# Kernel optimization log

Measured on AMD Instinct MI355X. Metric: run time of the kernel, lower is better.

The kernel has to match this reference:

```python
import jax, jax.numpy as jnp
import numpy as np

B, S, D_EMB, D_HEAD = 4, 4096, 1024, 64

def setup_inputs() -> dict:
    key = jax.random.key(0)
    kx, kq, kk, kv = jax.random.split(key, 4)
    x = jax.random.normal(kx, (B, S, D_EMB), dtype=jnp.float32)
    # Linear(d_emb -> d_head, bias=False); stored as [d_emb, d_head] so y = x @ W
    sc = 1.0 / np.sqrt(D_EMB)
    Wq = jax.random.normal(kq, (D_EMB, D_HEAD), dtype=jnp.float32) * sc
    Wk = jax.random.normal(kk, (D_EMB, D_HEAD), dtype=jnp.float32) * sc
    Wv = jax.random.normal(kv, (D_EMB, D_HEAD), dtype=jnp.float32) * sc
    return {"x": x, "Wq": Wq, "Wk": Wk, "Wv": Wv}

def reference(x, Wq, Wk, Wv):
    # x: [B, S, D_EMB]
    n = x.shape[1]
    d_head = Wq.shape[1]
    q = x @ Wq  # [B, S, d_head]
    k = x @ Wk
    v = x @ Wv
    w = jnp.einsum('bqd,bkd->bqk', q, k)  # raw scores [B, S, S]
    causal = jnp.tril(jnp.ones((n, n), dtype=bool))
    w = jnp.where(causal[None, :, :], w, -jnp.inf)
    # NOTE: original scales AFTER masking (-inf * scale stays -inf, so math matches SDPA)
    scale = jnp.asarray(d_head, w.dtype) ** -0.5
    w = jax.nn.softmax(w * scale, axis=-1)
    # dropout_p = 0.0 (eval-mode reference)
    return w @ v  # [B, S, d_head]
```

## Files before the change

kernel.cpp:

```cpp
#include <hip/hip_runtime.h>

typedef __attribute__((ext_vector_type(4))) float f32x4;
typedef __attribute__((ext_vector_type(8))) short bf16x8;

#define S_LEN 4096

__device__ inline short f2bf(float f) {
    union { float f; unsigned u; } v; v.f = f;
    unsigned r = (v.u + 0x7fffu + ((v.u >> 16) & 1u)) >> 16;
    return (short)r;
}
__device__ inline unsigned pack2bf(float a, float b) {
    return (unsigned)(unsigned short)f2bf(a) | ((unsigned)(unsigned short)f2bf(b) << 16);
}
__device__ inline unsigned cvt_pk_bf16(float lo, float hi) {
    unsigned r;
    asm("v_cvt_pk_bf16_f32 %0, %1, %2" : "=v"(r) : "v"(lo), "v"(hi));
    return r;
}
__device__ inline void gload_lds16(const void* g, void* l) {
    __builtin_amdgcn_global_load_lds(
        (const __attribute__((address_space(1))) unsigned int*)g,
        (__attribute__((address_space(3))) unsigned int*)l, 16, 0, 0);
}

__global__ __launch_bounds__(256) void wconv_kernel(const float* __restrict__ Wq,
        const float* __restrict__ Wk, const float* __restrict__ Wv,
        short* __restrict__ Wsz) {
    int idx = blockIdx.x * 256 + threadIdx.x;
    int t = idx / 6144;
    int rem = idx - t * 6144;
    int g = rem >> 5, kk = rem & 31;
    int k = t * 32 + kk;
    int m = g >> 6, c = g & 63;
    const float* W = (m == 0) ? Wq : (m == 1) ? Wk : Wv;
    Wsz[idx] = f2bf(W[k * 64 + c]);
}

__global__ __launch_bounds__(256, 4) void qkv_kernel(const float* __restrict__ x,
        const short* __restrict__ Wsz, short* __restrict__ Qb,
        short* __restrict__ Ksz, short* __restrict__ Vsz) {
    __shared__ __align__(16) char Bl[2][12288];
    const int tid = threadIdx.x;
    const int wv = tid >> 6, lane = tid & 63;
    const int wr = wv & 1, wc = wv >> 1;
    const int lr = lane & 15, lg = lane >> 4;
    const int rowbase = blockIdx.x * 32 + wr * 16;

    f32x4 acc[6];
#pragma unroll
    for (int i = 0; i < 6; i++) acc[i] = {0.f, 0.f, 0.f, 0.f};

    const float* xrow = x + (size_t)(rowbase + lr) * 1024 + lg * 8;
    const char* wsrc = (const char*)Wsz + tid * 16;

#define STAGEB(t_, buf_)                                                    \
    {                                                                       \
        const char* s_ = wsrc + (t_) * 12288;                               \
        char* d_ = &Bl[(buf_)][tid * 16];                                   \
        gload_lds16(s_,        d_);                                         \
        gload_lds16(s_ + 4096, d_ + 4096);                                  \
        gload_lds16(s_ + 8192, d_ + 8192);                                  \
    }

    STAGEB(0, 0);
    __syncthreads();

#pragma unroll 4
    for (int t = 0; t < 32; t++) {
        if (t + 1 < 32) STAGEB(t + 1, (t + 1) & 1);

        f32x4 a0 = *(const f32x4*)(xrow + t * 32);
        f32x4 a1 = *(const f32x4*)(xrow + t * 32 + 4);
        union { unsigned u[4]; bf16x8 v; } au;
        au.u[0] = cvt_pk_bf16(a0[0], a0[1]);
        au.u[1] = cvt_pk_bf16(a0[2], a0[3]);
        au.u[2] = cvt_pk_bf16(a1[0], a1[1]);
        au.u[3] = cvt_pk_bf16(a1[2], a1[3]);

        const char* Bb = &Bl[t & 1][0];
#pragma unroll
        for (int cf = 0; cf < 6; cf++) {
            int brow = wc * 96 + cf * 16 + lr;
            bf16x8 b = *(const bf16x8*)(Bb + brow * 64 + lg * 16);
            acc[cf] = __builtin_amdgcn_mfma_f32_16x16x32_bf16(au.v, b, acc[cf], 0, 0, 0);
        }
        __syncthreads();
    }
#undef STAGEB

#pragma unroll
    for (int cf = 0; cf < 6; cf++) {
        int gcol = wc * 96 + cf * 16 + lr;
        int m = gcol >> 6, cm = gcol & 63;
#pragma unroll
        for (int r = 0; r < 4; r++) {
            int row = rowbase + lg * 4 + r;
            short bv = f2bf(acc[cf][r]);
            if (m == 0) {
                Qb[(size_t)row * 64 + cm] = bv;
            } else if (m == 1) {
                int b = row >> 12, s12 = row & 4095;
                int tk = s12 >> 6, rr = s12 & 63;
                Ksz[(((size_t)(b * 64 + tk) * 64 + rr) << 6)
                    + (((cm >> 3) ^ (rr & 7)) << 3) + (cm & 7)] = bv;
            } else {
                int b = row >> 12, s12 = row & 4095;
                int tk = s12 >> 6, kk = s12 & 63;
                Vsz[(((size_t)(b * 64 + tk) * 64 + cm) << 6)
                    + (((kk >> 3) ^ (cm & 7)) << 3) + (kk & 7)] = bv;
            }
        }
    }
}

__global__ __launch_bounds__(256, 3) void attn_fused_kernel(const short* __restrict__ Qb,
        const short* __restrict__ Ksz, const short* __restrict__ Vsz,
        float* __restrict__ o_part, float* __restrict__ m_part, float* __restrict__ l_part) {
    __shared__ __align__(16) char kvb2[2][16384];
    __shared__ __align__(16) char Pl[4 * 4096];
    const int tid = threadIdx.x;
    const int wv = tid >> 6, lane = tid & 63;
    const int lr = lane & 15, lg = lane >> 4;

    const int j = blockIdx.x;
    const int bb = j / 272;
    int jb = j - bb * 272;
    int qt = 0;
    while (jb >= ((qt + 2) >> 1)) { jb -= (qt + 2) >> 1; qt++; }
    const int c = jb;
    const int t0 = c * 4;
    const int nb = min(4, 2 * qt + 2 - 4 * c);
    const int qb_w = qt * 128 + wv * 32;

    bf16x8 qa[2][2];
#pragma unroll
    for (int qf = 0; qf < 2; qf++)
#pragma unroll
        for (int dk = 0; dk < 2; dk++)
            qa[qf][dk] = *(const bf16x8*)(Qb + (size_t)(bb * S_LEN + qb_w + qf * 16 + lr) * 64 + dk * 32 + lg * 8);

    f32x4 o[2][4];
    float mrun[2] = {-1e30f, -1e30f}, lrun[2] = {0.f, 0.f};
#pragma unroll
    for (int qf = 0; qf < 2; qf++)
#pragma unroll
        for (int df = 0; df < 4; df++) o[qf][df] = {0.f, 0.f, 0.f, 0.f};

    const char* Kg = (const char*)Ksz;
    const char* Vg = (const char*)Vsz;
    char* Pb = Pl + wv * 4096;

#define STAGEKV(t_, s_)                                                       \
    {                                                                         \
        size_t off_ = (size_t)(bb * 64 + t0 + (t_)) * 8192 + tid * 16;        \
        char* d_ = kvb2[(s_)] + tid * 16;                                     \
        gload_lds16(Kg + off_,        d_);                                    \
        gload_lds16(Kg + off_ + 4096, d_ + 4096);                             \
        gload_lds16(Vg + off_,        d_ + 8192);                             \
        gload_lds16(Vg + off_ + 4096, d_ + 12288);                            \
    }

    STAGEKV(0, 0);
    asm volatile("s_waitcnt vmcnt(0)" ::: "memory");
    __builtin_amdgcn_s_barrier();

    for (int t = 0; t < nb; t++) {
        if (t + 1 < nb) STAGEKV(t + 1, (t + 1) & 1);

        const int kv0 = (t0 + t) * 64;
        if (kv0 <= qb_w + 31) {
            const char* Kl = kvb2[t & 1];
            const char* Vl = Kl + 8192;

            bf16x8 kb[4][2], vb[2][4];
#pragma unroll
            for (int kf = 0; kf < 4; kf++)
#pragma unroll
                for (int dk = 0; dk < 2; dk++) {
                    int r = kf * 16 + lr;
                    kb[kf][dk] = *(const bf16x8*)(Kl + r * 128 + ((((dk << 2) | lg) ^ (r & 7)) << 4));
                }
#pragma unroll
            for (int kk = 0; kk < 2; kk++)
#pragma unroll
                for (int df = 0; df < 4; df++) {
                    int d = df * 16 + lr;
                    vb[kk][df] = *(const bf16x8*)(Vl + d * 128 + ((((kk << 2) | lg) ^ (d & 7)) << 4));
                }

            f32x4 s[2][4];
#pragma unroll
            for (int qf = 0; qf < 2; qf++)
#pragma unroll
                for (int kf = 0; kf < 4; kf++) {
                    f32x4 z = {0.f, 0.f, 0.f, 0.f};
                    z = __builtin_amdgcn_mfma_f32_16x16x32_bf16(kb[kf][0], qa[qf][0], z, 0, 0, 0);
                    s[qf][kf] = __builtin_amdgcn_mfma_f32_16x16x32_bf16(kb[kf][1], qa[qf][1], z, 0, 0, 0);
                }

            const bool needmask = (kv0 + 63) > qb_w;
#pragma unroll
            for (int qf = 0; qf < 2; qf++)
#pragma unroll
                for (int kf = 0; kf < 4; kf++)
#pragma unroll
                    for (int r = 0; r < 4; r++) {
                        float v = s[qf][kf][r] * 0.125f;
                        if (needmask) {
                            int row = qb_w + qf * 16 + lr;
                            int col = kv0 + kf * 16 + lg * 4 + r;
                            if (col > row) v = -1e30f;
                        }
                        s[qf][kf][r] = v;
                    }

#pragma unroll
            for (int qf = 0; qf < 2; qf++) {
                float pm = -1e30f;
#pragma unroll
                for (int kf = 0; kf < 4; kf++)
#pragma unroll
                    for (int r = 0; r < 4; r++) pm = fmaxf(pm, s[qf][kf][r]);
                pm = fmaxf(pm, __shfl_xor(pm, 16, 64));
                pm = fmaxf(pm, __shfl_xor(pm, 32, 64));
                float mnew = fmaxf(mrun[qf], pm);
                float fac = __expf(mrun[qf] - mnew);
                mrun[qf] = mnew;

                const int q = qf * 16 + lr;
                const int swz = (q & 7) << 4;
                float rs = 0.f;
#pragma unroll
                for (int kf = 0; kf < 4; kf++) {
                    float p0 = __expf(s[qf][kf][0] - mnew);
                    float p1 = __expf(s[qf][kf][1] - mnew);
                    float p2 = __expf(s[qf][kf][2] - mnew);
                    float p3 = __expf(s[qf][kf][3] - mnew);
                    rs += (p0 + p1) + (p2 + p3);
                    uint2 w; w.x = pack2bf(p0, p1); w.y = pack2bf(p2, p3);
                    int byt = (q * 128 + kf * 32 + lg * 8) ^ swz;
                    *(uint2*)(Pb + byt) = w;
                }
                rs += __shfl_xor(rs, 16, 64);
                rs += __shfl_xor(rs, 32, 64);
                lrun[qf] = lrun[qf] * fac + rs;
#pragma unroll
                for (int df = 0; df < 4; df++)
#pragma unroll
                    for (int r = 0; r < 4; r++) o[qf][df][r] *= fac;
            }

            bf16x8 pa[2][2];
#pragma unroll
            for (int qf = 0; qf < 2; qf++)
#pragma unroll
                for (int kk = 0; kk < 2; kk++) {
                    int q = qf * 16 + lr;
                    int byt = (q * 128 + kk * 64 + lg * 16) ^ ((q & 7) << 4);
                    pa[qf][kk] = *(const bf16x8*)(Pb + byt);
                }

#pragma unroll
            for (int qf = 0; qf < 2; qf++)
#pragma unroll
                for (int df = 0; df < 4; df++) {
                    o[qf][df] = __builtin_amdgcn_mfma_f32_16x16x32_bf16(vb[0][df], pa[qf][0], o[qf][df], 0, 0, 0);
                    o[qf][df] = __builtin_amdgcn_mfma_f32_16x16x32_bf16(vb[1][df], pa[qf][1], o[qf][df], 0, 0, 0);
                }
        }

        asm volatile("s_waitcnt vmcnt(0)" ::: "memory");
        __builtin_amdgcn_sched_barrier(0);
        __builtin_amdgcn_s_barrier();
    }
#undef STAGEKV

#pragma unroll
    for (int qf = 0; qf < 2; qf++)
#pragma unroll
        for (int df = 0; df < 4; df++)
            *(f32x4*)(o_part + ((size_t)j * 128 + wv * 32 + qf * 16 + lr) * 64 + df * 16 + lg * 4) = o[qf][df];
    if (lg == 0) {
#pragma unroll
        for (int qf = 0; qf < 2; qf++) {
            m_part[(size_t)j * 128 + wv * 32 + qf * 16 + lr] = mrun[qf];
            l_part[(size_t)j * 128 + wv * 32 + qf * 16 + lr] = lrun[qf];
        }
    }
}

__global__ __launch_bounds__(256) void combine_kernel(const float* __restrict__ o_part,
        const float* __restrict__ m_part, const float* __restrict__ l_part,
        float* __restrict__ out) {
    const int idx = blockIdx.x * 256 + threadIdx.x;
    const int col = idx & 63;
    const int rowg = idx >> 6;
    const int bb = rowg >> 12;
    const int srow = rowg & 4095;
    const int qt = srow >> 7;
    const int rloc = srow & 127;
    const int h = qt >> 1;
    const int n = (qt + 2) >> 1;
    const int jb0 = bb * 272 + h * (h + 1) + (qt & 1) * (h + 1);

    float M = -1e30f;
    for (int cc = 0; cc < n; cc++) M = fmaxf(M, m_part[(size_t)(jb0 + cc) * 128 + rloc]);
    float L = 0.f, acc = 0.f;
    for (int cc = 0; cc < n; cc++) {
        float w = __expf(m_part[(size_t)(jb0 + cc) * 128 + rloc] - M);
        L += l_part[(size_t)(jb0 + cc) * 128 + rloc] * w;
        acc += o_part[((size_t)(jb0 + cc) * 128 + rloc) * 64 + col] * w;
    }
    out[idx] = acc / L;
}

extern "C" void kernel_launch(void* const* d_in, const int* in_sizes, int n_in,
                              void* d_out, int out_size, void* d_ws, size_t ws_size,
                              hipStream_t stream) {
    const float* x  = (const float*)d_in[0];
    const float* Wq = (const float*)d_in[1];
    const float* Wk = (const float*)d_in[2];
    const float* Wv = (const float*)d_in[3];
    float* out = (float*)d_out;

    char* ws = (char*)d_ws;
    short* Wsz = (short*)(ws);
    short* Qb  = (short*)(ws + 0x60000);
    short* Ksz = (short*)(ws + 0x260000);
    short* Vsz = (short*)(ws + 0x460000);

    const int njobs = 1088;
    float* o_part = (float*)(ws + 0x660000);
    float* m_part = o_part + (size_t)njobs * 128 * 64;
    float* l_part = m_part + (size_t)njobs * 128;

    hipLaunchKernelGGL(wconv_kernel, dim3(768), dim3(256), 0, stream, Wq, Wk, Wv, Wsz);
    hipLaunchKernelGGL(qkv_kernel,  dim3(512), dim3(256), 0, stream, x, Wsz, Qb, Ksz, Vsz);
    hipLaunchKernelGGL(attn_fused_kernel, dim3(njobs), dim3(256), 0, stream,
                       Qb, Ksz, Vsz, o_part, m_part, l_part);
    hipLaunchKernelGGL(combine_kernel, dim3(4096), dim3(256), 0, stream,
                       o_part, m_part, l_part, out);
}
```

Baseline: 82.61 us.

## Stage x tiles through LDS with triple-buffered async loads in QKV projection

The QKV projection kernel now stages the fp32 x tile into LDS with global_load_lds, using an XOR swizzle, alongside the weight tile. It uses a three-deep buffer ring with a prefetch distance of two, and replaces __syncthreads with explicit vmcnt waits plus a single barrier per iteration. The aim is to hide global load latency for the activation reads, which were previously direct per-lane global loads on the critical path. In exchange, LDS use grows to 48KB per block and the occupancy hint drops from 4 to 2 blocks.

```diff
diff --git a/kernel.cpp b/kernel.cpp
--- a/kernel.cpp
+++ b/kernel.cpp
@@ -37,57 +37,69 @@
     Wsz[idx] = f2bf(W[k * 64 + c]);
 }
 
-__global__ __launch_bounds__(256, 4) void qkv_kernel(const float* __restrict__ x,
+__global__ __launch_bounds__(256, 2) void qkv_kernel(const float* __restrict__ x,
         const short* __restrict__ Wsz, short* __restrict__ Qb,
         short* __restrict__ Ksz, short* __restrict__ Vsz) {
-    __shared__ __align__(16) char Bl[2][12288];
+    __shared__ __align__(16) char lds[3][16384];
     const int tid = threadIdx.x;
     const int wv = tid >> 6, lane = tid & 63;
     const int wr = wv & 1, wc = wv >> 1;
     const int lr = lane & 15, lg = lane >> 4;
-    const int rowbase = blockIdx.x * 32 + wr * 16;
+    const int rowbase = blockIdx.x * 32;
 
     f32x4 acc[6];
 #pragma unroll
     for (int i = 0; i < 6; i++) acc[i] = {0.f, 0.f, 0.f, 0.f};
 
-    const float* xrow = x + (size_t)(rowbase + lr) * 1024 + lg * 8;
+    const int arow = tid >> 3, acL = tid & 7;
+    const char* asrc = (const char*)(x + (size_t)(rowbase + arow) * 1024
+                                     + ((acL ^ (arow & 7)) << 2));
     const char* wsrc = (const char*)Wsz + tid * 16;
 
-#define STAGEB(t_, buf_)                                                    \
+#define STAGE(t_, s_)                                                       \
     {                                                                       \
-        const char* s_ = wsrc + (t_) * 12288;                               \
-        char* d_ = &Bl[(buf_)][tid * 16];                                   \
-        gload_lds16(s_,        d_);                                         \
-        gload_lds16(s_ + 4096, d_ + 4096);                                  \
-        gload_lds16(s_ + 8192, d_ + 8192);                                  \
-    }
-
-    STAGEB(0, 0);
-    __syncthreads();
-
-#pragma unroll 4
+        char* base_ = lds[(s_)];                                            \
+        gload_lds16(asrc + (t_) * 128, base_ + tid * 16);                   \
+        const char* bs_ = wsrc + (t_) * 12288;                              \
+        gload_lds16(bs_,        base_ + 4096 + tid * 16);                   \
+        gload_lds16(bs_ + 4096, base_ + 8192 + tid * 16);                   \
+        gload_lds16(bs_ + 8192, base_ + 12288 + tid * 16);                  \
+    }
+
+    STAGE(0, 0);
+    STAGE(1, 1);
+
+    const int rowA = wr * 16 + lr;
+    const int aswz = rowA & 7;
+
+#pragma unroll
     for (int t = 0; t < 32; t++) {
-        if (t + 1 < 32) STAGEB(t + 1, (t + 1) & 1);
-
-        f32x4 a0 = *(const f32x4*)(xrow + t * 32);
-        f32x4 a1 = *(const f32x4*)(xrow + t * 32 + 4);
+        if (t < 31) asm volatile("s_waitcnt vmcnt(4)" ::: "memory");
+        else        asm volatile("s_waitcnt vmcnt(0)" ::: "memory");
+        __builtin_amdgcn_sched_barrier(0);
+        __builtin_amdgcn_s_barrier();
+        __builtin_amdgcn_sched_barrier(0);
+        if (t + 2 < 32) STAGE(t + 2, (t + 2) % 3);
+
+        const char* Ab = lds[t % 3];
+        const char* Bb = lds[t % 3] + 4096;
+
+        f32x4 a0 = *(const f32x4*)(Ab + rowA * 128 + (((lg * 2) ^ aswz) << 4));
+        f32x4 a1 = *(const f32x4*)(Ab + rowA * 128 + (((lg * 2 + 1) ^ aswz) << 4));
         union { unsigned u[4]; bf16x8 v; } au;
         au.u[0] = cvt_pk_bf16(a0[0], a0[1]);
         au.u[1] = cvt_pk_bf16(a0[2], a0[3]);
         au.u[2] = cvt_pk_bf16(a1[0], a1[1]);
         au.u[3] = cvt_pk_bf16(a1[2], a1[3]);
 
-        const char* Bb = &Bl[t & 1][0];
 #pragma unroll
         for (int cf = 0; cf < 6; cf++) {
             int brow = wc * 96 + cf * 16 + lr;
             bf16x8 b = *(const bf16x8*)(Bb + brow * 64 + lg * 16);
             acc[cf] = __builtin_amdgcn_mfma_f32_16x16x32_bf16(au.v, b, acc[cf], 0, 0, 0);
         }
-        __syncthreads();
-    }
-#undef STAGEB
+    }
+#undef STAGE
 
 #pragma unroll
     for (int cf = 0; cf < 6; cf++) {
@@ -95,7 +107,7 @@
         int m = gcol >> 6, cm = gcol & 63;
 #pragma unroll
         for (int r = 0; r < 4; r++) {
-            int row = rowbase + lg * 4 + r;
+            int row = rowbase + wr * 16 + lg * 4 + r;
             short bv = f2bf(acc[cf][r]);
             if (m == 0) {
                 Qb[(size_t)row * 64 + cm] = bv;
```

After: 71.33 us. 13.7% less time.
